# Optimization experiments

Hardware: AMD Instinct MI355X
Metric: run time of the kernel (lower is better)

## Reference

```python
import jax, jax.numpy as jnp
import numpy as np

P_SIZE = 13
B_THRESH = 1.3  # |u| >= b -> hard 1.0
N_POW = 64      # u^n / (u^n + 1)


def make_dct_weight(p):
    idx = np.arange(p)
    Ci = np.where(idx == 0, 1.0 / np.sqrt(2.0), 1.0)
    cos = np.cos((2 * idx[:, None] + 1) * idx[None, :] * np.pi / (2 * p)) * Ci[None, :]  # [x,i]
    P = (2.0 / p) * np.einsum('xi,yj->xyij', cos, cos).reshape(p * p, p * p)
    return P.T.astype(np.float32).reshape(p * p, 1, p, p)


def conv2d(x, w, padding):
    return jax.lax.conv_general_dilated(x, w, (1, 1), padding,
                                        dimension_numbers=('NCHW', 'OIHW', 'NCHW'))


def udiff(u):
    # x^64/(x^64+1), saturated to 1 for |x| >= 1.3 (even power, sign-safe)
    au = jnp.abs(u)
    us = jnp.where(au < B_THRESH, u, 0.0)  # avoid overflow in pow
    y = us ** N_POW
    return jnp.where(au >= B_THRESH, jnp.ones_like(u), y / (y + 1.0))


def setup_inputs() -> dict:
    key = jax.random.key(0)
    k1, _ = jax.random.split(key)
    x = jax.random.uniform(k1, (2, 1, 512, 512), dtype=jnp.float32)
    sigma = jnp.full((1,), 0.1, dtype=jnp.float32)
    W_dct = jnp.asarray(make_dct_weight(P_SIZE))  # [p^2, 1, p, p], learnable in original
    return {"x": x, "sigma": sigma, "W_dct": W_dct}


def reference(x, sigma, W_dct):
    N, _, H, W = x.shape
    p = W_dct.shape[-1]
    pp = p * p
    # patch DCT: [N, p^2, H-p+1, W-p+1]
    t = conv2d(x, W_dct, 'VALID')
    nz = udiff(t / (3.0 * sigma))
    y = t * nz
    w = 1.0 / (1.0 + jnp.sum(nz, axis=1, keepdims=True))  # [N,1,H',W']
    # inverse transform as 1x1 conv with inv(dct matrix)
    Minv = jnp.linalg.inv(W_dct.reshape(pp, pp))
    z = jnp.einsum('kc,nchw->nkhw', Minv, y)
    z = w * z
    # overlap-add fold == conv with spatially-flipped identity patch kernel, full padding
    fold_k = jnp.flip(jnp.eye(pp, dtype=x.dtype).reshape(pp, p, p), axis=(1, 2))[None]  # [1,p^2,p,p]
    folded = conv2d(z, fold_k, [(p - 1, p - 1), (p - 1, p - 1)])  # [N,1,H,W]
    out = folded[:, :, p - 1:H - (p - 1), p - 1:W - (p - 1)]
    divisor = conv2d(w, jnp.ones((1, 1, p, p), x.dtype), 'VALID')
    return out / divisor
```

## Files before the change

kernel.cpp:

```cpp
#include <hip/hip_runtime.h>
#include <math.h>


#define P13    13
#define IMGW   512
#define OUTW   488
#define SEGH   61
#define NSEG   8
#define HCOLS  512
#define HPITCH 16

struct C1mat { float v[P13 * P13]; };

constexpr double kPI = 3.14159265358979323846264338327950288;

constexpr double ccos_pm_pi(double th) {
    double term = 1.0, s = 1.0;
    const double th2 = th * th;
    for (int n = 1; n <= 25; ++n) {
        term *= -th2 / (double)((2 * n - 1) * (2 * n));
        s += term;
    }
    return s;
}
constexpr double csqrt(double v) {
    double x = (v > 1.0) ? v : 1.0;
    for (int i = 0; i < 64; ++i) x = 0.5 * (x + v / x);
    return x;
}
constexpr C1mat make_c1() {
    C1mat m{};
    const double s213 = csqrt(2.0 / 13.0);
    const double is2  = 1.0 / csqrt(2.0);
    for (int x = 0; x < P13; ++x)
        for (int k = 0; k < P13; ++k) {
            int mm = ((2 * x + 1) * k) % 52;
            double th = (mm <= 26) ? (mm * kPI / 26.0) : ((mm - 52) * kPI / 26.0);
            double Ci = (k == 0) ? is2 : 1.0;
            m.v[x * P13 + k] = (float)(s213 * Ci * ccos_pm_pi(th));
        }
    return m;
}
__device__ constexpr C1mat c1c = make_c1();

#define ROR16_ADD(v, N)                                                        \
    v += __int_as_float(__builtin_amdgcn_mov_dpp(__float_as_int(v),            \
                                                 0x120 + (N), 0xF, 0xF, true))

__device__ __forceinline__ void vdct_shrink(const float (&Rv)[P13],
                                            float inv3s, float (&tn)[P13], float& pnz)
{
    float Se[6], So[6];
#pragma unroll
    for (int k = 0; k < 6; ++k) { Se[k] = Rv[k] + Rv[12 - k]; So[k] = Rv[k] - Rv[12 - k]; }
#pragma unroll
    for (int i = 0; i < P13; ++i) {
        float t;
        if ((i & 1) == 0) {
            t = c1c.v[6 * P13 + i] * Rv[6];
#pragma unroll
            for (int k = 0; k < 6; ++k) t = fmaf(c1c.v[k * P13 + i], Se[k], t);
        } else {
            t = c1c.v[0 * P13 + i] * So[0];
#pragma unroll
            for (int k = 1; k < 6; ++k) t = fmaf(c1c.v[k * P13 + i], So[k], t);
        }
        float u = t * inv3s;
        u = __builtin_amdgcn_fmed3f(u, -1.3f, 1.3f);
        float lg  = __builtin_amdgcn_logf(fabsf(u));
        float p64 = __builtin_amdgcn_exp2f(64.0f * lg);
        float nz  = p64 * __builtin_amdgcn_rcpf(p64 + 1.0f);
        pnz += nz;
        tn[i] = t * nz;
    }
}

__device__ __forceinline__ void fold_vert(const float (&tn)[P13], float w1, float (&H)[P13])
{
#pragma unroll
    for (int dx = 0; dx < 6; ++dx) {
        float E = c1c.v[dx * P13 + 0] * tn[0];
#pragma unroll
        for (int i = 2; i < P13; i += 2) E = fmaf(c1c.v[dx * P13 + i], tn[i], E);
        float O = c1c.v[dx * P13 + 1] * tn[1];
#pragma unroll
        for (int i = 3; i < P13; i += 2) O = fmaf(c1c.v[dx * P13 + i], tn[i], O);
        H[dx]      = fmaf(w1, E + O, H[dx]);
        H[12 - dx] = fmaf(w1, E - O, H[12 - dx]);
    }
    float z6 = c1c.v[6 * P13 + 0] * tn[0];
#pragma unroll
    for (int i = 2; i < P13; i += 2) z6 = fmaf(c1c.v[6 * P13 + i], tn[i], z6);
    H[6] = fmaf(w1, z6, H[6]);
}

__global__ __launch_bounds__(256) void dct2net_k2(
    const float* __restrict__ xg, const float* __restrict__ sigmag,
    float* __restrict__ Hg, float* __restrict__ Wg)
{
    __shared__ float c1lds[169];
    const int tid = threadIdx.x;
    if (tid < 169) c1lds[tid] = c1c.v[tid];
    __syncthreads();

    const int lane = tid & 63;
    const int wv   = tid >> 6;
    const int g    = lane >> 4;
    const int jj   = lane & 15;
    const int img  = blockIdx.z;
    const int hs   = blockIdx.y * SEGH;
    const int cbw  = blockIdx.x * 16 + wv * 4;
    const int col  = cbw + g;

    const float inv3s = 1.0f / (3.0f * sigmag[0]);
    const float* xin  = xg + (size_t)img * IMGW * IMGW;

    float c1col[P13];
    {
        const int jc = (jj < 13) ? jj : 12;
#pragma unroll
        for (int y = 0; y < P13; ++y) c1col[y] = c1lds[y * P13 + jc];
    }

    float Rv[P13], Hr[P13];
#pragma unroll
    for (int k = 0; k < P13; ++k) { Rv[k] = 0.0f; Hr[k] = 0.0f; }

    int xcol = cbw + lane; xcol = (xcol < IMGW - 1) ? xcol : (IMGW - 1);
    float xv = 0.0f;
    if (lane < 16) xv = xin[(size_t)hs * IMGW + xcol];

    for (int k = 0; k <= 84; ++k) {
        float xw[P13];
#pragma unroll
        for (int y = 0; y < P13; ++y)
            xw[y] = __int_as_float(
                __builtin_amdgcn_ds_bpermute(4 * (g + y), __float_as_int(xv)));
        {
            int nr = hs + k + 1; nr = (nr < IMGW) ? nr : (IMGW - 1);
            if (lane < 16) xv = xin[(size_t)nr * IMGW + xcol];
        }
        float a0 = c1col[0] * xw[0], a1 = c1col[1] * xw[1];
#pragma unroll
        for (int y = 2; y < P13; y += 2) a0 = fmaf(c1col[y], xw[y], a0);
#pragma unroll
        for (int y = 3; y < P13; y += 2) a1 = fmaf(c1col[y], xw[y], a1);
#pragma unroll
        for (int q = 0; q < P13 - 1; ++q) Rv[q] = Rv[q + 1];
        Rv[P13 - 1] = a0 + a1;

        if (k >= 12) {
            const int ph = hs + k - 12;
            float tn[P13]; float pnz = 0.0f;
            vdct_shrink(Rv, inv3s, tn, pnz);
            if (jj >= 13) pnz = 0.0f;
            ROR16_ADD(pnz, 1);
            ROR16_ADD(pnz, 2);
            ROR16_ADD(pnz, 4);
            ROR16_ADD(pnz, 8);
            const float w = __builtin_amdgcn_rcpf(1.0f + pnz);
            if (jj == 0) Wg[((size_t)img * IMGW + ph) * IMGW + col] = w;
            fold_vert(tn, w, Hr);
            if (k >= 24) {
                const int a = hs + k - 24;
                Hg[(((size_t)img * OUTW + a) * HCOLS + col) * HPITCH + jj] = Hr[0];
            }
#pragma unroll
            for (int q = 0; q < P13 - 1; ++q) Hr[q] = Hr[q + 1];
            Hr[P13 - 1] = 0.0f;
        }
    }
}

__global__ __launch_bounds__(256) void dct2net_k3(
    const float* __restrict__ Hg, const float* __restrict__ Wg,
    float* __restrict__ outg)
{
    __shared__ float U[4][76][14];
    __shared__ float vw[4][80];
    const int tid  = threadIdx.x;
    const int lane = tid & 63;
    const int wv   = tid >> 6;
    const int img  = blockIdx.z;
    const int a    = blockIdx.y * 4 + wv;
    const int cb   = blockIdx.x * 64;

#pragma unroll
    for (int h = 0; h < 2; ++h) {
        const int li = lane + 64 * h;
        if (h == 0 || lane < 12) {
            int c = cb + li; c = (c < 499) ? c : 499;
            const float* hp = &Hg[(((size_t)img * OUTW + a) * HCOLS + c) * HPITCH];
            float hv[P13];
            *(float4*)&hv[0] = *(const float4*)hp;
            *(float4*)&hv[4] = *(const float4*)(hp + 4);
            *(float4*)&hv[8] = *(const float4*)(hp + 8);
            hv[12] = hp[12];
#pragma unroll
            for (int dy = 0; dy < P13; ++dy) {
                float s0 = c1c.v[dy * P13 + 0] * hv[0];
                float s1 = c1c.v[dy * P13 + 1] * hv[1];
#pragma unroll
                for (int j = 2; j < P13; j += 2) s0 = fmaf(c1c.v[dy * P13 + j], hv[j], s0);
#pragma unroll
                for (int j = 3; j < P13; j += 2) s1 = fmaf(c1c.v[dy * P13 + j], hv[j], s1);
                U[wv][li][dy] = s0 + s1;
            }
            float s = 0.0f;
            const float* wp = &Wg[((size_t)img * IMGW + a) * IMGW + c];
#pragma unroll
            for (int dx = 0; dx < P13; ++dx) s += wp[dx * IMGW];
            vw[wv][li] = s;
        }
    }
    float num = 0.0f;
#pragma unroll
    for (int dy = 0; dy < P13; ++dy) num += U[wv][lane + 12 - dy][dy];
    float den = 0.0f;
#pragma unroll
    for (int d = 0; d < P13; ++d) den += vw[wv][lane + d];
    const int ow = cb + lane;
    if (ow < OUTW)
        outg[((size_t)img * OUTW + a) * OUTW + ow] = num * __builtin_amdgcn_rcpf(den);
}

extern "C" void kernel_launch(void* const* d_in, const int* in_sizes, int n_in,
                              void* d_out, int out_size, void* d_ws, size_t ws_size,
                              hipStream_t stream)
{
    const float* x     = (const float*)d_in[0];
    const float* sigma = (const float*)d_in[1];
    float* out = (float*)d_out;

    float* Hg = (float*)d_ws;
    float* Wg = Hg + (size_t)2 * OUTW * HCOLS * HPITCH;

    dct2net_k2<<<dim3(32, NSEG, 2), 256, 0, stream>>>(x, sigma, Hg, Wg);
    dct2net_k3<<<dim3(8, 122, 2), 256, 0, stream>>>(Hg, Wg, out);
}
```

Baseline: 178.8 us.

## Split rows into more segments, peel loop phases, precompute vertical weight sums

```diff
diff --git a/kernel.cpp b/kernel.cpp
--- a/kernel.cpp
+++ b/kernel.cpp
@@ -5,8 +5,8 @@
 #define P13    13
 #define IMGW   512
 #define OUTW   488
-#define SEGH   61
-#define NSEG   8
+#define SEGH   31
+#define NSEG   16
 #define HCOLS  512
 #define HPITCH 16
 
@@ -43,6 +43,9 @@
 }
 __device__ constexpr C1mat c1c = make_c1();
 
+struct FalseT { static constexpr bool value = false; };
+struct TrueT  { static constexpr bool value = true; };
+
 #define ROR16_ADD(v, N)                                                        \
     v += __int_as_float(__builtin_amdgcn_mov_dpp(__float_as_int(v),            \
                                                  0x120 + (N), 0xF, 0xF, true))
@@ -66,10 +69,9 @@
             for (int k = 1; k < 6; ++k) t = fmaf(c1c.v[k * P13 + i], So[k], t);
         }
         float u = t * inv3s;
-        u = __builtin_amdgcn_fmed3f(u, -1.3f, 1.3f);
-        float lg  = __builtin_amdgcn_logf(fabsf(u));
-        float p64 = __builtin_amdgcn_exp2f(64.0f * lg);
-        float nz  = p64 * __builtin_amdgcn_rcpf(p64 + 1.0f);
+        float lg = __builtin_amdgcn_logf(fabsf(u));
+        float q  = __builtin_amdgcn_exp2f(-64.0f * lg);
+        float nz = __builtin_amdgcn_rcpf(1.0f + q);
         pnz += nz;
         tn[i] = t * nz;
     }
@@ -109,6 +111,7 @@
     const int jj   = lane & 15;
     const int img  = blockIdx.z;
     const int hs   = blockIdx.y * SEGH;
+    const int segrows = (OUTW - hs < SEGH) ? (OUTW - hs) : SEGH;
     const int cbw  = blockIdx.x * 16 + wv * 4;
     const int col  = cbw + g;
 
@@ -122,15 +125,18 @@
         for (int y = 0; y < P13; ++y) c1col[y] = c1lds[y * P13 + jc];
     }
 
-    float Rv[P13], Hr[P13];
+    float Rv[P13], Hr[P13], wr[12];
 #pragma unroll
     for (int k = 0; k < P13; ++k) { Rv[k] = 0.0f; Hr[k] = 0.0f; }
+#pragma unroll
+    for (int k = 0; k < 12; ++k) wr[k] = 0.0f;
+    float vs = 0.0f;
 
     int xcol = cbw + lane; xcol = (xcol < IMGW - 1) ? xcol : (IMGW - 1);
     float xv = 0.0f;
     if (lane < 16) xv = xin[(size_t)hs * IMGW + xcol];
 
-    for (int k = 0; k <= 84; ++k) {
+    auto step = [&](int k, auto SH, auto RT) {
         float xw[P13];
 #pragma unroll
         for (int y = 0; y < P13; ++y)
@@ -149,8 +155,7 @@
         for (int q = 0; q < P13 - 1; ++q) Rv[q] = Rv[q + 1];
         Rv[P13 - 1] = a0 + a1;
 
-        if (k >= 12) {
-            const int ph = hs + k - 12;
+        if constexpr (decltype(SH)::value) {
             float tn[P13]; float pnz = 0.0f;
             vdct_shrink(Rv, inv3s, tn, pnz);
             if (jj >= 13) pnz = 0.0f;
@@ -159,17 +164,30 @@
             ROR16_ADD(pnz, 4);
             ROR16_ADD(pnz, 8);
             const float w = __builtin_amdgcn_rcpf(1.0f + pnz);
-            if (jj == 0) Wg[((size_t)img * IMGW + ph) * IMGW + col] = w;
+            vs += w;
             fold_vert(tn, w, Hr);
-            if (k >= 24) {
+            if constexpr (decltype(RT)::value) {
                 const int a = hs + k - 24;
                 Hg[(((size_t)img * OUTW + a) * HCOLS + col) * HPITCH + jj] = Hr[0];
+                if (jj == 0) Wg[((size_t)img * IMGW + a) * IMGW + col] = vs;
+                vs -= wr[0];
             }
+#pragma unroll
+            for (int q = 0; q < 11; ++q) wr[q] = wr[q + 1];
+            wr[11] = w;
 #pragma unroll
             for (int q = 0; q < P13 - 1; ++q) Hr[q] = Hr[q + 1];
             Hr[P13 - 1] = 0.0f;
         }
-    }
+    };
+
+#pragma unroll 4
+    for (int k = 0; k < 12; ++k) step(k, FalseT{}, FalseT{});
+#pragma unroll 4
+    for (int k = 12; k < 24; ++k) step(k, TrueT{}, FalseT{});
+    const int kend = 24 + segrows;
+#pragma unroll 4
+    for (int k = 24; k < kend; ++k) step(k, TrueT{}, TrueT{});
 }
 
 __global__ __launch_bounds__(256) void dct2net_k3(
@@ -196,6 +214,7 @@
             *(float4*)&hv[4] = *(const float4*)(hp + 4);
             *(float4*)&hv[8] = *(const float4*)(hp + 8);
             hv[12] = hp[12];
+            vw[wv][li] = Wg[((size_t)img * IMGW + a) * IMGW + c];
 #pragma unroll
             for (int dy = 0; dy < P13; ++dy) {
                 float s0 = c1c.v[dy * P13 + 0] * hv[0];
@@ -206,11 +225,6 @@
                 for (int j = 3; j < P13; j += 2) s1 = fmaf(c1c.v[dy * P13 + j], hv[j], s1);
                 U[wv][li][dy] = s0 + s1;
             }
-            float s = 0.0f;
-            const float* wp = &Wg[((size_t)img * IMGW + a) * IMGW + c];
-#pragma unroll
-            for (int dx = 0; dx < P13; ++dx) s += wp[dx * IMGW];
-            vw[wv][li] = s;
         }
     }
     float num = 0.0f;
```

Result: no change. 179.9 us (+0.6%).
